# Optimization experiments

Hardware: AMD Instinct MI355X
Metric: run time of the kernel (lower is better)

The kernel has to match this reference:

```python
import jax, jax.numpy as jnp
import numpy as np

D_MODEL, D_STATE, D_CONV, EXPAND = 512, 16, 4, 2
D_INNER = EXPAND * D_MODEL
DT_RANK = -(-D_MODEL // 16)  # ceil(512/16) = 32
B, L = 1, 2048


def setup_inputs() -> dict:
    key = jax.random.key(0)
    ks = jax.random.split(key, 10)
    x = jax.random.normal(ks[0], (B, L, D_MODEL), dtype=jnp.float32)
    in_proj_w = jax.random.normal(ks[1], (2 * D_INNER, D_MODEL), dtype=jnp.float32) * (D_MODEL ** -0.5)
    conv_w = jax.random.normal(ks[2], (D_INNER, 1, D_CONV), dtype=jnp.float32) * (D_CONV ** -0.5)
    conv_b = jax.random.normal(ks[3], (D_INNER,), dtype=jnp.float32) * 0.02
    x_proj_w = jax.random.normal(ks[4], (DT_RANK + 2 * D_STATE, D_INNER), dtype=jnp.float32) * (D_INNER ** -0.5)
    dt_init_std = DT_RANK ** -0.5
    dt_proj_w = jax.random.uniform(ks[5], (D_INNER, DT_RANK), minval=-dt_init_std, maxval=dt_init_std, dtype=jnp.float32)
    # dt bias init: inverse-softplus of dt sampled log-uniform in [dt_min, dt_max]
    dt = jnp.exp(jax.random.uniform(ks[6], (D_INNER,)) * (np.log(0.1) - np.log(0.001)) + np.log(0.001))
    dt = jnp.clip(dt, 1e-4, None)
    dt_proj_b = dt + jnp.log(-jnp.expm1(-dt))
    A_log = jnp.log(jnp.broadcast_to(jnp.arange(1, D_STATE + 1, dtype=jnp.float32), (D_INNER, D_STATE)))
    D = jnp.ones((D_INNER,), dtype=jnp.float32)
    out_proj_w = jax.random.normal(ks[7], (D_MODEL, D_INNER), dtype=jnp.float32) * (D_INNER ** -0.5)
    return {"x": x, "in_proj_w": in_proj_w, "conv_w": conv_w, "conv_b": conv_b,
            "x_proj_w": x_proj_w, "dt_proj_w": dt_proj_w, "dt_proj_b": dt_proj_b,
            "A_log": A_log, "D": D, "out_proj_w": out_proj_w}


def _selective_scan_parallel(x, deltaA, deltaB, C):
    # x: (B,L,D)  deltaA/deltaB: (B,L,D,N)  C: (B,L,N)
    log_dA = jnp.log(jnp.clip(deltaA, 1e-6, None))
    cum_dA = jnp.exp(jnp.cumsum(log_dA, axis=1))                      # (B,L,D,N)
    Bx = deltaB * x[..., None]                                        # (B,L,D,N)
    cum_dA_prev = jnp.concatenate([jnp.ones_like(cum_dA[:, :1]), cum_dA[:, :-1]], axis=1)
    h = cum_dA * jnp.cumsum(Bx / (cum_dA_prev + 1e-8), axis=1)        # (B,L,D,N)
    return jnp.einsum('bldn,bln->bld', h, C)


def reference(x, in_proj_w, conv_w, conv_b, x_proj_w, dt_proj_w, dt_proj_b, A_log, D, out_proj_w):
    xz = jnp.einsum('bld,ed->ble', x, in_proj_w)            # (B,L,2*D_inner)
    xp, z = jnp.split(xz, 2, axis=-1)
    # causal depthwise conv1d: left-pad d_conv-1, groups = d_inner
    xc = jax.lax.conv_general_dilated(
        jnp.transpose(xp, (0, 2, 1)), conv_w, window_strides=(1,),
        padding=[(D_CONV - 1, 0)], dimension_numbers=('NCH', 'OIH', 'NCH'),
        feature_group_count=D_INNER) + conv_b[None, :, None]
    xp = jax.nn.silu(jnp.transpose(xc, (0, 2, 1)))          # (B,L,D_inner)
    # SSM
    A = -jnp.exp(A_log.astype(jnp.float32))                 # (D_inner, N)
    x_dbl = jnp.einsum('bld,ed->ble', xp, x_proj_w)
    delta, Bm, Cm = jnp.split(x_dbl, [DT_RANK, DT_RANK + D_STATE], axis=-1)
    delta = jax.nn.softplus(jnp.einsum('blr,dr->bld', delta, dt_proj_w) + dt_proj_b)
    deltaA = jnp.exp(delta[..., None] * A)                  # (B,L,D,N)
    deltaB = delta[..., None] * Bm[:, :, None, :]           # (B,L,D,N)
    y = _selective_scan_parallel(xp, deltaA, deltaB, Cm)
    y = y + xp * D
    out = y * jax.nn.silu(z)
    return jnp.einsum('bld,md->blm', out, out_proj_w)
```

## Files before the change

### kernel.cpp

```cpp
#include <hip/hip_runtime.h>
#include <hip/hip_bf16.h>

#define L_SEQ   2048
#define D_MODEL 512
#define D_INNER 1024
#define D_STATE 16
#define DT_RANK 32

typedef unsigned short u16;
typedef short bf16x8 __attribute__((ext_vector_type(8)));
typedef float f32x4  __attribute__((ext_vector_type(4)));
typedef unsigned short u16x8 __attribute__((ext_vector_type(8)));

__device__ __forceinline__ u16 f2bf(float f) {
    union { float f; unsigned u; } x; x.f = f;
    unsigned r = x.u + 0x7FFFu + ((x.u >> 16) & 1u);
    return (u16)(r >> 16);
}

__device__ __forceinline__ void gload_lds16(const void* g, void* l) {
    __builtin_amdgcn_global_load_lds((const __attribute__((address_space(1))) void*)g,
                                     (__attribute__((address_space(3))) void*)l, 16, 0, 0);
}

template<int BM, int BN>
__global__ __launch_bounds__(256)
void gemm_mfma_nt(const u16* __restrict__ A, const u16* __restrict__ B,
                  float* __restrict__ C, int M, int N, int K, int ldc) {
    constexpr int FM = BM / 32;
    constexpr int FN = BN / 32;
    __shared__ u16 lA[BM * 64];
    __shared__ u16 lB[BN * 64];

    const int tid  = threadIdx.x;
    const int lane = tid & 63;
    const int w    = tid >> 6;
    const int wr   = w >> 1, wc = w & 1;
    const int m0 = blockIdx.y * BM;
    const int n0 = blockIdx.x * BN;

    f32x4 acc[FM][FN];
#pragma unroll
    for (int m = 0; m < FM; m++)
#pragma unroll
        for (int n = 0; n < FN; n++) acc[m][n] = (f32x4){0.f, 0.f, 0.f, 0.f};

    int offA[FM][2], offB[FN][2];
#pragma unroll
    for (int m = 0; m < FM; m++) {
        int r = wr * (BM / 2) + m * 16 + (lane & 15);
#pragma unroll
        for (int s = 0; s < 2; s++) {
            int kb = s * 4 + (lane >> 4);
            offA[m][s] = r * 128 + ((kb ^ (r & 7)) << 4);
        }
    }
#pragma unroll
    for (int n = 0; n < FN; n++) {
        int r = wc * (BN / 2) + n * 16 + (lane & 15);
#pragma unroll
        for (int s = 0; s < 2; s++) {
            int kb = s * 4 + (lane >> 4);
            offB[n][s] = r * 128 + ((kb ^ (r & 7)) << 4);
        }
    }

    const int ldsbase = (tid & 192) * 16;

    for (int k0 = 0; k0 < K; k0 += 64) {
        __syncthreads();
#pragma unroll
        for (int i = 0; i < BM / 32; i++) {
            int o = i * 4096 + tid * 16;
            int r = o >> 7;
            int kb = ((o >> 4) & 7) ^ (r & 7);
            gload_lds16(A + (size_t)(m0 + r) * K + k0 + kb * 8,
                        (char*)lA + i * 4096 + ldsbase);
        }
#pragma unroll
        for (int i = 0; i < BN / 32; i++) {
            int o = i * 4096 + tid * 16;
            int r = o >> 7;
            int kb = ((o >> 4) & 7) ^ (r & 7);
            gload_lds16(B + (size_t)(n0 + r) * K + k0 + kb * 8,
                        (char*)lB + i * 4096 + ldsbase);
        }
        __syncthreads();

#pragma unroll
        for (int s = 0; s < 2; s++) {
            bf16x8 av[FM], bv[FN];
#pragma unroll
            for (int m = 0; m < FM; m++)
                av[m] = *(const bf16x8*)((const char*)lA + offA[m][s]);
#pragma unroll
            for (int n = 0; n < FN; n++)
                bv[n] = *(const bf16x8*)((const char*)lB + offB[n][s]);
#pragma unroll
            for (int m = 0; m < FM; m++)
#pragma unroll
                for (int n = 0; n < FN; n++)
                    acc[m][n] = __builtin_amdgcn_mfma_f32_16x16x32_bf16(
                        av[m], bv[n], acc[m][n], 0, 0, 0);
        }
    }

    const int rb = (lane >> 4) * 4;
    const int cb = lane & 15;
#pragma unroll
    for (int m = 0; m < FM; m++)
#pragma unroll
        for (int n = 0; n < FN; n++) {
            int col = n0 + wc * (BN / 2) + n * 16 + cb;
#pragma unroll
            for (int j = 0; j < 4; j++) {
                int row = m0 + wr * (BM / 2) + m * 16 + rb + j;
                C[(size_t)row * ldc + col] = acc[m][n][j];
            }
        }
}

__global__ __launch_bounds__(256)
void cast3_kernel(const float* __restrict__ x, const float* __restrict__ w1,
                  const float* __restrict__ w2,
                  u16* __restrict__ xb, u16* __restrict__ w1b, u16* __restrict__ w2b) {
    int g = blockIdx.x * 256 + threadIdx.x;
    const float* src; u16* dst; int off;
    if (g < 131072)      { src = x;  dst = xb;  off = g; }
    else if (g < 262144) { src = w1; dst = w1b; off = g - 131072; }
    else                 { src = w2; dst = w2b; off = g - 262144; }
    float4 v0 = ((const float4*)src)[off * 2];
    float4 v1 = ((const float4*)src)[off * 2 + 1];
    u16x8 r;
    r[0] = f2bf(v0.x); r[1] = f2bf(v0.y); r[2] = f2bf(v0.z); r[3] = f2bf(v0.w);
    r[4] = f2bf(v1.x); r[5] = f2bf(v1.y); r[6] = f2bf(v1.z); r[7] = f2bf(v1.w);
    *(u16x8*)(dst + (size_t)off * 8) = r;
}

__global__ __launch_bounds__(256)
void conv_rows_kernel(const float* __restrict__ xzT,
                      const float* __restrict__ w,
                      const float* __restrict__ b,
                      float* __restrict__ xpcT) {
    const int d = blockIdx.y;
    const int l = blockIdx.x * 1024 + threadIdx.x * 4;
    const float4 wv = ((const float4*)w)[d];
    const float bias = b[d];
    const float* row = xzT + (size_t)d * L_SEQ;

    float4 cur  = *(const float4*)(row + l);
    float4 prev = (l == 0) ? make_float4(0.f, 0.f, 0.f, 0.f)
                           : *(const float4*)(row + l - 4);
    float e1 = prev.y, e2 = prev.z, e3 = prev.w;
    float e4 = cur.x, e5 = cur.y, e6 = cur.z, e7 = cur.w;
    float4 r;
    r.x = bias + wv.x * e1 + wv.y * e2 + wv.z * e3 + wv.w * e4;
    r.y = bias + wv.x * e2 + wv.y * e3 + wv.z * e4 + wv.w * e5;
    r.z = bias + wv.x * e3 + wv.y * e4 + wv.z * e5 + wv.w * e6;
    r.w = bias + wv.x * e4 + wv.y * e5 + wv.z * e6 + wv.w * e7;
    r.x = r.x / (1.f + __expf(-r.x));
    r.y = r.y / (1.f + __expf(-r.y));
    r.z = r.z / (1.f + __expf(-r.z));
    r.w = r.w / (1.f + __expf(-r.w));
    *(float4*)(xpcT + (size_t)d * L_SEQ + l) = r;
}

__global__ __launch_bounds__(256)
void xproj_kernel(const float* __restrict__ xpcT,
                  const float* __restrict__ xw,
                  float* __restrict__ xdblT) {
    const int tid  = threadIdx.x;
    const int part = tid >> 7;
    const int e    = (tid >> 1) & 63;
    const int lc   = tid & 1;
    const int l0   = blockIdx.x * 8;

    const float* wrow = xw + (size_t)e * 1024 + part * 512;
    const float* xcol = xpcT + (size_t)part * 512 * L_SEQ + l0 + lc * 4;

    f32x4 acc = {0.f, 0.f, 0.f, 0.f};
#pragma unroll 4
    for (int k = 0; k < 512; k += 4) {
        float4 wv = *(const float4*)(wrow + k);
        f32x4 x0 = *(const f32x4*)(xcol + (size_t)(k + 0) * L_SEQ);
        f32x4 x1 = *(const f32x4*)(xcol + (size_t)(k + 1) * L_SEQ);
        f32x4 x2 = *(const f32x4*)(xcol + (size_t)(k + 2) * L_SEQ);
        f32x4 x3 = *(const f32x4*)(xcol + (size_t)(k + 3) * L_SEQ);
        acc += wv.x * x0 + wv.y * x1 + wv.z * x2 + wv.w * x3;
    }

    __shared__ f32x4 red[128];
    if (part == 1) red[(e << 1) | lc] = acc;
    __syncthreads();
    if (part == 0) {
        acc += red[(e << 1) | lc];
        *(f32x4*)(xdblT + (size_t)e * L_SEQ + l0 + lc * 4) = acc;
    }
}

__global__ __launch_bounds__(256)
void deltaT_kernel(const float* __restrict__ xdblT,
                   const float* __restrict__ dtw,
                   const float* __restrict__ dtb,
                   float* __restrict__ deltaT) {
    const int tid = threadIdx.x;
    const int d0 = blockIdx.x * 64;
    const int l0 = blockIdx.y * 128;

    __shared__ float sx[32][128];
#pragma unroll
    for (int it = 0; it < 4; it++) {
        int idx = it * 256 + tid;
        int r  = idx >> 5;
        int c4 = (idx & 31) * 4;
        *(float4*)&sx[r][c4] = *(const float4*)(xdblT + (size_t)r * 2048 + l0 + c4);
    }

    const int dl = tid >> 2;
    const int lg = tid & 3;
    const int d  = d0 + dl;
    float wreg[32];
#pragma unroll
    for (int r4 = 0; r4 < 32; r4 += 4)
        *(float4*)&wreg[r4] = *(const float4*)(dtw + (size_t)d * 32 + r4);
    const float bias = dtb[d];
    __syncthreads();

#pragma unroll
    for (int j = 0; j < 8; j++) {
        float4 a = make_float4(bias, bias, bias, bias);
        const int col = j * 16 + lg * 4;
#pragma unroll
        for (int r = 0; r < 32; r++) {
            float4 v = *(const float4*)&sx[r][col];
            a.x = fmaf(wreg[r], v.x, a.x);
            a.y = fmaf(wreg[r], v.y, a.y);
            a.z = fmaf(wreg[r], v.z, a.z);
            a.w = fmaf(wreg[r], v.w, a.w);
        }
        float4 o;
        o.x = fmaxf(a.x, 0.f) + log1pf(expf(-fabsf(a.x)));
        o.y = fmaxf(a.y, 0.f) + log1pf(expf(-fabsf(a.y)));
        o.z = fmaxf(a.z, 0.f) + log1pf(expf(-fabsf(a.z)));
        o.w = fmaxf(a.w, 0.f) + log1pf(expf(-fabsf(a.w)));
        *(float4*)(deltaT + (size_t)d * 2048 + l0 + col) = o;
    }
}

#define NCHUNK 32

__global__ __launch_bounds__(1024)
void scan_kernel(const float* __restrict__ deltaT,
                 const float* __restrict__ xpcT,
                 const float* __restrict__ xzT,
                 const float* __restrict__ xdblT,
                 const float* __restrict__ A_log, const float* __restrict__ Dv,
                 u16* __restrict__ ypreT) {
    const int tid   = threadIdx.x;
    const int lane  = tid & 63;
    const int chunk = ((tid >> 6) << 1) | (lane >> 5);
    const int dl    = (lane >> 4) & 1;
    const int n     = lane & 15;
    const int li    = (dl << 4) | n;
    const int d0    = blockIdx.x * 2;
    const int d     = d0 + dl;
    const int lb    = chunk * 64;

    const float Aneg = -__expf(A_log[d * D_STATE + n]);

    const f32x4* dT4 = (const f32x4*)(deltaT + (size_t)d * L_SEQ + lb);
    const f32x4* xT4 = (const f32x4*)(xpcT   + (size_t)d * L_SEQ + lb);
    const f32x4* bT4 = (const f32x4*)(xdblT + (size_t)(32 + n) * L_SEQ + lb);
    const f32x4* cT4 = (const f32x4*)(xdblT + (size_t)(48 + n) * L_SEQ + lb);

    __shared__ float sLog[NCHUNK][32];
    __shared__ float sP[NCHUNK][32];
    __shared__ float sH[NCHUNK][32];
    __shared__ float s_p[2][NCHUNK][68];

    const float clipLog = -13.815511f;
    float s = 0.f;
#pragma unroll 8
    for (int i = 0; i < 16; i++) {
        f32x4 d4 = dT4[i];
#pragma unroll
        for (int k = 0; k < 4; k++) s += fmaxf(d4[k] * Aneg, clipLog);
    }
    sLog[chunk][li] = s;
    sP[chunk][li]   = __expf(s);
    __syncthreads();

    float lsum = 0.f;
    for (int v = 0; v < chunk; v++) lsum += sLog[v][li];
    const float cAs = __expf(lsum);

    float hloc = 0.f, cA = cAs;
    for (int i = 0; i < 16; i++) {
        f32x4 d4 = dT4[i], x4 = xT4[i], b4 = bT4[i];
#pragma unroll
        for (int k = 0; k < 4; k++) {
            float dA = fmaxf(__expf(d4[k] * Aneg), 1e-6f);
            float g  = cA * __builtin_amdgcn_rcpf(cA + 1e-8f);
            hloc = dA * hloc + (dA * g) * (d4[k] * b4[k] * x4[k]);
            cA *= dA;
        }
    }
    sH[chunk][li] = hloc;
    __syncthreads();

    float h = 0.f;
    for (int v = 0; v < chunk; v++) h = sP[v][li] * h + sH[v][li];

    cA = cAs;
    for (int i = 0; i < 16; i++) {
        f32x4 d4 = dT4[i], x4 = xT4[i], b4 = bT4[i], c4 = cT4[i];
#pragma unroll
        for (int k = 0; k < 4; k++) {
            float dA = fmaxf(__expf(d4[k] * Aneg), 1e-6f);
            float g  = cA * __builtin_amdgcn_rcpf(cA + 1e-8f);
            h  = dA * h + (dA * g) * (d4[k] * b4[k] * x4[k]);
            cA *= dA;
            float p = h * c4[k];
            p += __shfl_xor(p, 1);
            p += __shfl_xor(p, 2);
            p += __shfl_xor(p, 4);
            p += __shfl_xor(p, 8);
            if (n == 0) s_p[dl][chunk][4 * i + k] = p;
        }
    }
    __syncthreads();

    {
        const int rdl = tid >> 9;
        const int pos = (tid & 511) * 4;
        const int ck = pos >> 6, off = pos & 63;
        const float Ddr = Dv[d0 + rdl];
        f32x4 p4 = *(const f32x4*)&s_p[rdl][ck][off];
        f32x4 x4 = *(const f32x4*)(xpcT + (size_t)(d0 + rdl) * L_SEQ + pos);
        f32x4 z4 = *(const f32x4*)(xzT + (size_t)(1024 + d0 + rdl) * L_SEQ + pos);
        float y0 = (p4[0] + x4[0] * Ddr) * (z4[0] * __builtin_amdgcn_rcpf(1.f + __expf(-z4[0])));
        float y1 = (p4[1] + x4[1] * Ddr) * (z4[1] * __builtin_amdgcn_rcpf(1.f + __expf(-z4[1])));
        float y2 = (p4[2] + x4[2] * Ddr) * (z4[2] * __builtin_amdgcn_rcpf(1.f + __expf(-z4[2])));
        float y3 = (p4[3] + x4[3] * Ddr) * (z4[3] * __builtin_amdgcn_rcpf(1.f + __expf(-z4[3])));
        ushort4 o;
        o.x = f2bf(y0); o.y = f2bf(y1); o.z = f2bf(y2); o.w = f2bf(y3);
        *(ushort4*)(ypreT + (size_t)(d0 + rdl) * L_SEQ + pos) = o;
    }
}

__global__ __launch_bounds__(256)
void trans_bf16_kernel(const u16* __restrict__ src, u16* __restrict__ dst) {
    __shared__ u16 t[64][72];
    const int d0 = blockIdx.x * 64, l0 = blockIdx.y * 64;
    const int r = threadIdx.x >> 3;
    const int c = (threadIdx.x & 7) * 8;
#pragma unroll
    for (int rr = r; rr < 64; rr += 32)
        *(u16x8*)&t[rr][c] = *(const u16x8*)(src + (size_t)(d0 + rr) * L_SEQ + l0 + c);
    __syncthreads();
#pragma unroll
    for (int rr = r; rr < 64; rr += 32) {
        u16x8 v;
#pragma unroll
        for (int j = 0; j < 8; j++) v[j] = t[c + j][rr];
        *(u16x8*)(dst + (size_t)(l0 + rr) * D_INNER + d0 + c) = v;
    }
}

extern "C" void kernel_launch(void* const* d_in, const int* in_sizes, int n_in,
                              void* d_out, int out_size, void* d_ws, size_t ws_size,
                              hipStream_t stream) {
    const float* x          = (const float*)d_in[0];
    const float* in_proj_w  = (const float*)d_in[1];
    const float* conv_w     = (const float*)d_in[2];
    const float* conv_b     = (const float*)d_in[3];
    const float* x_proj_w   = (const float*)d_in[4];
    const float* dt_proj_w  = (const float*)d_in[5];
    const float* dt_proj_b  = (const float*)d_in[6];
    const float* A_log      = (const float*)d_in[7];
    const float* Dv         = (const float*)d_in[8];
    const float* out_proj_w = (const float*)d_in[9];
    float* out = (float*)d_out;
    float* ws  = (float*)d_ws;

    float* xzT    = ws;
    float* xpcT   = ws + 4194304;
    float* xdblT  = ws + 6291456;
    float* deltaT = ws + 6422528;
    u16*   ypreT  = (u16*)(ws + 8519680);
    u16*   ypre   = (u16*)(ws + 9568256);
    u16*   xb     = (u16*)(ws + 10616832);
    u16*   w1b    = (u16*)(ws + 11141120);
    u16*   w2b    = (u16*)(ws + 11665408);

    cast3_kernel<<<1280, 256, 0, stream>>>(x, in_proj_w, out_proj_w, xb, w1b, w2b);

    gemm_mfma_nt<64, 64><<<dim3(2048 / 64, 2048 / 64), 256, 0, stream>>>(
        w1b, xb, xzT, 2 * D_INNER, L_SEQ, D_MODEL, L_SEQ);

    conv_rows_kernel<<<dim3(2, 1024), 256, 0, stream>>>(xzT, conv_w, conv_b, xpcT);

    xproj_kernel<<<256, 256, 0, stream>>>(xpcT, x_proj_w, xdblT);

    deltaT_kernel<<<dim3(16, 16), 256, 0, stream>>>(xdblT, dt_proj_w, dt_proj_b,
                                                    deltaT);

    scan_kernel<<<512, 1024, 0, stream>>>(deltaT, xpcT, xzT, xdblT,
                                          A_log, Dv, ypreT);

    trans_bf16_kernel<<<dim3(16, 32), 256, 0, stream>>>(ypreT, ypre);

    gemm_mfma_nt<64, 32><<<dim3(512 / 32, 2048 / 64), 256, 0, stream>>>(
        ypre, w2b, out, L_SEQ, D_MODEL, D_INNER, D_MODEL);
}
```

Measured before the change: 156.1 us.

## Reformulate chunked selective scan as prefix sums to break serial dependencies

Replaces the recurrent h = dA*h + ... update inside each chunk with an explicit prefix-sum form. The cumulative decay is taken as exp of a running log-sum, and the state is carry-decay times a running sum of scaled inputs. This turns the long serial FMA chain into independent per-element work with short 4-wide prefix adds, so more instruction-level parallelism is available. It also removes the sP/sH shared arrays and the cross-chunk h recurrence, and the four shuffle reductions are interleaved. The cost is extra exp evaluations per element, and rounding differs from the reference because of the running log-sum and the 1/cumA scaling.

```diff
diff --git a/kernel.cpp b/kernel.cpp
--- a/kernel.cpp
+++ b/kernel.cpp
@@ -274,58 +274,108 @@
     const f32x4* cT4 = (const f32x4*)(xdblT + (size_t)(48 + n) * L_SEQ + lb);
 
     __shared__ float sLog[NCHUNK][32];
-    __shared__ float sP[NCHUNK][32];
-    __shared__ float sH[NCHUNK][32];
+    __shared__ float sU[NCHUNK][32];
     __shared__ float s_p[2][NCHUNK][68];
 
     const float clipLog = -13.815511f;
-    float s = 0.f;
-#pragma unroll 8
+    const float EPS = 1e-8f;
+
+    float sa0 = 0.f, sa1 = 0.f, sa2 = 0.f, sa3 = 0.f;
     for (int i = 0; i < 16; i++) {
         f32x4 d4 = dT4[i];
-#pragma unroll
-        for (int k = 0; k < 4; k++) s += fmaxf(d4[k] * Aneg, clipLog);
-    }
-    sLog[chunk][li] = s;
-    sP[chunk][li]   = __expf(s);
+        sa0 += fmaxf(d4[0] * Aneg, clipLog);
+        sa1 += fmaxf(d4[1] * Aneg, clipLog);
+        sa2 += fmaxf(d4[2] * Aneg, clipLog);
+        sa3 += fmaxf(d4[3] * Aneg, clipLog);
+    }
+    sLog[chunk][li] = (sa0 + sa1) + (sa2 + sa3);
     __syncthreads();
 
     float lsum = 0.f;
     for (int v = 0; v < chunk; v++) lsum += sLog[v][li];
-    const float cAs = __expf(lsum);
-
-    float hloc = 0.f, cA = cAs;
-    for (int i = 0; i < 16; i++) {
-        f32x4 d4 = dT4[i], x4 = xT4[i], b4 = bT4[i];
-#pragma unroll
-        for (int k = 0; k < 4; k++) {
-            float dA = fmaxf(__expf(d4[k] * Aneg), 1e-6f);
-            float g  = cA * __builtin_amdgcn_rcpf(cA + 1e-8f);
-            hloc = dA * hloc + (dA * g) * (d4[k] * b4[k] * x4[k]);
-            cA *= dA;
-        }
-    }
-    sH[chunk][li] = hloc;
-    __syncthreads();
-
-    float h = 0.f;
-    for (int v = 0; v < chunk; v++) h = sP[v][li] * h + sH[v][li];
-
-    cA = cAs;
-    for (int i = 0; i < 16; i++) {
-        f32x4 d4 = dT4[i], x4 = xT4[i], b4 = bT4[i], c4 = cT4[i];
-#pragma unroll
-        for (int k = 0; k < 4; k++) {
-            float dA = fmaxf(__expf(d4[k] * Aneg), 1e-6f);
-            float g  = cA * __builtin_amdgcn_rcpf(cA + 1e-8f);
-            h  = dA * h + (dA * g) * (d4[k] * b4[k] * x4[k]);
-            cA *= dA;
-            float p = h * c4[k];
-            p += __shfl_xor(p, 1);
-            p += __shfl_xor(p, 2);
-            p += __shfl_xor(p, 4);
-            p += __shfl_xor(p, 8);
-            if (n == 0) s_p[dl][chunk][4 * i + k] = p;
+
+    {
+        float carry = lsum;
+        float ec = __expf(carry);
+        float U0 = 0.f, U1 = 0.f, U2 = 0.f, U3 = 0.f;
+        for (int i = 0; i < 16; i++) {
+            f32x4 d4 = dT4[i], x4 = xT4[i], b4 = bT4[i];
+            float l0 = fmaxf(d4[0] * Aneg, clipLog);
+            float l1 = fmaxf(d4[1] * Aneg, clipLog);
+            float l2 = fmaxf(d4[2] * Aneg, clipLog);
+            float l3 = fmaxf(d4[3] * Aneg, clipLog);
+            float t01 = l0 + l1;
+            float p0 = l0, p1 = t01, p2 = t01 + l2, p3 = t01 + (l2 + l3);
+            float ca0 = __expf(carry + p0);
+            float ca1 = __expf(carry + p1);
+            float ca2 = __expf(carry + p2);
+            float ca3 = __expf(carry + p3);
+            float i0 = d4[0] * b4[0] * x4[0];
+            float i1 = d4[1] * b4[1] * x4[1];
+            float i2 = d4[2] * b4[2] * x4[2];
+            float i3 = d4[3] * b4[3] * x4[3];
+            U0 += i0 * __builtin_amdgcn_rcpf(ec  + EPS);
+            U1 += i1 * __builtin_amdgcn_rcpf(ca0 + EPS);
+            U2 += i2 * __builtin_amdgcn_rcpf(ca1 + EPS);
+            U3 += i3 * __builtin_amdgcn_rcpf(ca2 + EPS);
+            carry += p3;
+            ec = ca3;
+        }
+        sU[chunk][li] = (U0 + U1) + (U2 + U3);
+    }
+    __syncthreads();
+
+    float Sc = 0.f;
+    for (int v = 0; v < chunk; v++) Sc += sU[v][li];
+
+    {
+        float carry = lsum;
+        float ec = __expf(carry);
+        for (int i = 0; i < 16; i++) {
+            f32x4 d4 = dT4[i], x4 = xT4[i], b4 = bT4[i], c4 = cT4[i];
+            float l0 = fmaxf(d4[0] * Aneg, clipLog);
+            float l1 = fmaxf(d4[1] * Aneg, clipLog);
+            float l2 = fmaxf(d4[2] * Aneg, clipLog);
+            float l3 = fmaxf(d4[3] * Aneg, clipLog);
+            float t01 = l0 + l1;
+            float p0 = l0, p1 = t01, p2 = t01 + l2, p3 = t01 + (l2 + l3);
+            float ca0 = __expf(carry + p0);
+            float ca1 = __expf(carry + p1);
+            float ca2 = __expf(carry + p2);
+            float ca3 = __expf(carry + p3);
+            float i0 = d4[0] * b4[0] * x4[0];
+            float i1 = d4[1] * b4[1] * x4[1];
+            float i2 = d4[2] * b4[2] * x4[2];
+            float i3 = d4[3] * b4[3] * x4[3];
+            float u0 = i0 * __builtin_amdgcn_rcpf(ec  + EPS);
+            float u1 = i1 * __builtin_amdgcn_rcpf(ca0 + EPS);
+            float u2 = i2 * __builtin_amdgcn_rcpf(ca1 + EPS);
+            float u3 = i3 * __builtin_amdgcn_rcpf(ca2 + EPS);
+            float q01 = u0 + u1;
+            float s0 = u0, s1 = q01, s2 = q01 + u2, s3 = q01 + (u2 + u3);
+            float h0 = ca0 * (Sc + s0);
+            float h1 = ca1 * (Sc + s1);
+            float h2 = ca2 * (Sc + s2);
+            float h3 = ca3 * (Sc + s3);
+            float pv0 = h0 * c4[0], pv1 = h1 * c4[1];
+            float pv2 = h2 * c4[2], pv3 = h3 * c4[3];
+            pv0 += __shfl_xor(pv0, 1); pv0 += __shfl_xor(pv0, 2);
+            pv0 += __shfl_xor(pv0, 4); pv0 += __shfl_xor(pv0, 8);
+            pv1 += __shfl_xor(pv1, 1); pv1 += __shfl_xor(pv1, 2);
+            pv1 += __shfl_xor(pv1, 4); pv1 += __shfl_xor(pv1, 8);
+            pv2 += __shfl_xor(pv2, 1); pv2 += __shfl_xor(pv2, 2);
+            pv2 += __shfl_xor(pv2, 4); pv2 += __shfl_xor(pv2, 8);
+            pv3 += __shfl_xor(pv3, 1); pv3 += __shfl_xor(pv3, 2);
+            pv3 += __shfl_xor(pv3, 4); pv3 += __shfl_xor(pv3, 8);
+            if (n == 0) {
+                s_p[dl][chunk][4 * i + 0] = pv0;
+                s_p[dl][chunk][4 * i + 1] = pv1;
+                s_p[dl][chunk][4 * i + 2] = pv2;
+                s_p[dl][chunk][4 * i + 3] = pv3;
+            }
+            Sc += s3;
+            carry += p3;
+            ec = ca3;
         }
     }
     __syncthreads();
```

Measured after the change: 161.0 us. +3.2%, slower.
